# Kernel optimization log

Measured on AMD Instinct MI355X. Metric: run time of the kernel, lower is better.

The kernel has to match this reference:

```python
import jax, jax.numpy as jnp
import numpy as np

B, T, C = 4, 2048, 1024
H = 16
D = C // H  # head_dim = 64


def setup_inputs() -> dict:
    key = jax.random.key(0)
    k1, k2, k3 = jax.random.split(key, 3)
    x = jax.random.normal(k1, (B, T, C), dtype=jnp.float32)
    w_qkv = jax.random.normal(k2, (C, 3 * C), dtype=jnp.float32) * (C ** -0.5)
    b_qkv = jnp.zeros((3 * C,), dtype=jnp.float32)
    w_proj = jax.random.normal(k3, (C, C), dtype=jnp.float32) * (C ** -0.5)
    b_proj = jnp.zeros((C,), dtype=jnp.float32)
    return {"x": x, "w_qkv": w_qkv, "b_qkv": b_qkv, "w_proj": w_proj, "b_proj": b_proj}


def reference(x, w_qkv, b_qkv, w_proj, b_proj):
    # qkv projection: (B,T,C) -> (B,T,3,H,D) -> q,k,v each (B,H,T,D)
    qkv = (x @ w_qkv + b_qkv).reshape(B, T, 3, H, D)
    q, k, v = jnp.moveaxis(qkv, 2, 0)           # each (B, T, H, D)
    q = q.transpose(0, 2, 1, 3)                 # (B, H, T, D)
    k = k.transpose(0, 2, 1, 3)
    v = v.transpose(0, 2, 1, 3)

    scale = 1.0 / jnp.sqrt(jnp.float32(D))
    attn = jnp.einsum('bhqd,bhkd->bhqk', q, k) * scale  # (B,H,T,T)
    causal = jnp.tril(jnp.ones((T, T), dtype=bool))
    attn = jnp.where(causal[None, None], attn, -jnp.inf)
    attn = jax.nn.softmax(attn, axis=-1)
    # dropout p=0.0 (eval mode) -> identity
    out = jnp.einsum('bhqk,bhkd->bhqd', attn, v)        # (B,H,T,D)
    out = out.transpose(0, 2, 1, 3).reshape(B, T, C)
    return out @ w_proj + b_proj
```

## Files before the change

kernel.cpp:

```cpp
#include <hip/hip_runtime.h>
#include <hip/hip_bf16.h>


#define Bsz 4
#define Tsz 2048
#define Csz 1024
#define Hn  16
#define Dh  64

typedef unsigned short u16;
typedef __attribute__((ext_vector_type(8))) short bf16x8;
typedef __attribute__((ext_vector_type(4))) float f32x4;
typedef __attribute__((ext_vector_type(4))) unsigned int u32x4;
typedef __attribute__((ext_vector_type(2))) unsigned int u32x2;

__device__ __forceinline__ u16 f2b(float f) {
  __hip_bfloat16 h = __float2bfloat16(f);
  return *reinterpret_cast<u16*>(&h);
}

__device__ __forceinline__ unsigned pk2(float lo, float hi) {
  return __builtin_amdgcn_perm(__float_as_uint(hi) + 0x8000u,
                               __float_as_uint(lo) + 0x8000u, 0x07060302u);
}

#if __has_builtin(__builtin_amdgcn_exp2f)
#define EX2(x) __builtin_amdgcn_exp2f(x)
#else
#define EX2(x) exp2f(x)
#endif

__device__ __forceinline__ void gld_lds16(const void* g, void* lds) {
  __builtin_amdgcn_global_load_lds(
      (const __attribute__((address_space(1))) unsigned int*)g,
      (__attribute__((address_space(3))) unsigned int*)lds, 16, 0, 0);
}

__global__ __launch_bounds__(256) void cvt_f32_bf16(const float* __restrict__ in,
                                                    u16* __restrict__ out) {
  size_t i = ((size_t)blockIdx.x * 256 + threadIdx.x) * 8;
  f32x4 a = *(const f32x4*)(in + i);
  f32x4 b = *(const f32x4*)(in + i + 4);
  u16 r[8];
#pragma unroll
  for (int j = 0; j < 4; ++j) { r[j] = f2b(a[j]); r[4 + j] = f2b(b[j]); }
  *(u32x4*)(out + i) = *(const u32x4*)r;
}

__global__ __launch_bounds__(256) void cvt_transpose(const float* __restrict__ in,
                                                     u16* __restrict__ out,
                                                     int R, int C) {
  __shared__ u16 tile[64 * 66];
  const int r0 = blockIdx.x * 64, c0 = blockIdx.y * 64;
  const int tid = threadIdx.x;
#pragma unroll
  for (int i = 0; i < 16; ++i) {
    int idx = i * 256 + tid;
    int r = idx >> 6, c = idx & 63;
    tile[r * 66 + c] = f2b(in[(size_t)(r0 + r) * C + (c0 + c)]);
  }
  __syncthreads();
#pragma unroll
  for (int i = 0; i < 16; ++i) {
    int idx = i * 256 + tid;
    int c = idx >> 6, r = idx & 63;
    out[(size_t)(c0 + c) * R + (r0 + r)] = tile[r * 66 + c];
  }
}

__device__ __forceinline__ void gemm_tile_acc(const u16* __restrict__ A,
                                              const u16* __restrict__ Bt,
                                              int m0, int n0,
                                              u16* Als, u16* Bls,
                                              f32x4 acc[4][2]) {
  const int tid = threadIdx.x;
  const int w = tid >> 6, lane = tid & 63;
  const int wm = w & 1, wn = w >> 1;
  const int col = lane & 15, quad = lane >> 4;
#pragma unroll
  for (int mt = 0; mt < 4; ++mt)
#pragma unroll
    for (int nt = 0; nt < 2; ++nt)
      acc[mt][nt] = (f32x4){0.f, 0.f, 0.f, 0.f};

  const u16* asrc[2];
  const u16* bsrc[2];
#pragma unroll
  for (int c = 0; c < 2; ++c) {
    int slot = c * 512 + tid;
    int trow = slot >> 3, seg = slot & 7;
    size_t off = (size_t)trow * 1024 + (size_t)((seg ^ (trow & 7)) * 8);
    asrc[c] = A + (size_t)m0 * 1024 + off;
    bsrc[c] = Bt + (size_t)n0 * 1024 + off;
  }
  const int swz = col & 7;
  const int o0 = ((0 + quad) ^ swz) * 8;
  const int o1 = ((4 + quad) ^ swz) * 8;

#pragma unroll
  for (int c = 0; c < 2; ++c) {
    gld_lds16(asrc[c], (char*)Als + (size_t)(c * 512 + w * 64) * 16);
    gld_lds16(bsrc[c], (char*)Bls + (size_t)(c * 512 + w * 64) * 16);
    asrc[c] += 64; bsrc[c] += 64;
  }

  const int nkt = 1024 / 64;
  for (int t = 0; t < nkt; ++t) {
    asm volatile("s_waitcnt vmcnt(0)" ::: "memory");
    __builtin_amdgcn_s_barrier();
    __builtin_amdgcn_sched_barrier(0);
    const int cur = t & 1;
    if (t + 1 < nkt) {
      const int nxt = cur ^ 1;
      u16* Ad = Als + nxt * 8192;
      u16* Bd = Bls + nxt * 8192;
#pragma unroll
      for (int c = 0; c < 2; ++c) {
        gld_lds16(asrc[c], (char*)Ad + (size_t)(c * 512 + w * 64) * 16);
        gld_lds16(bsrc[c], (char*)Bd + (size_t)(c * 512 + w * 64) * 16);
        asrc[c] += 64; bsrc[c] += 64;
      }
    }
    const u16* Ac = Als + cur * 8192;
    const u16* Bc = Bls + cur * 8192;
    bf16x8 af[4][2], bfr[2][2];
#pragma unroll
    for (int mt = 0; mt < 4; ++mt) {
      const u16* r = Ac + (size_t)(wm * 64 + mt * 16 + col) * 64;
      af[mt][0] = *(const bf16x8*)(r + o0);
      af[mt][1] = *(const bf16x8*)(r + o1);
    }
#pragma unroll
    for (int nt = 0; nt < 2; ++nt) {
      const u16* r = Bc + (size_t)(wn * 32 + nt * 16 + col) * 64;
      bfr[nt][0] = *(const bf16x8*)(r + o0);
      bfr[nt][1] = *(const bf16x8*)(r + o1);
    }
#pragma unroll
    for (int kk = 0; kk < 2; ++kk)
#pragma unroll
      for (int mt = 0; mt < 4; ++mt)
#pragma unroll
        for (int nt = 0; nt < 2; ++nt)
          acc[mt][nt] = __builtin_amdgcn_mfma_f32_16x16x32_bf16(
              af[mt][kk], bfr[nt][kk], acc[mt][nt], 0, 0, 0);
  }
}

__global__ __launch_bounds__(512, 4) void gemm_qkv(const u16* __restrict__ X,
                                                   const u16* __restrict__ WT,
                                                   const float* __restrict__ bias,
                                                   u16* __restrict__ Q,
                                                   u16* __restrict__ Kc,
                                                   u16* __restrict__ Vt) {
  __shared__ __align__(16) u16 Als[2 * 128 * 64];
  __shared__ __align__(16) u16 Bls[2 * 128 * 64];
  f32x4 acc[4][2];
  const int m0 = blockIdx.x * 128, n0 = blockIdx.y * 128;
  gemm_tile_acc(X, WT, m0, n0, Als, Bls, acc);

  const float qscale = 0.18033688011112042f;
  const int tid = threadIdx.x;
  const int w = tid >> 6, lane = tid & 63;
  const int wm = w & 1, wn = w >> 1;
  const int col = lane & 15, quad = lane >> 4;
#pragma unroll
  for (int mt = 0; mt < 4; ++mt)
#pragma unroll
    for (int nt = 0; nt < 2; ++nt) {
      int n = n0 + wn * 32 + nt * 16 + col;
      int s = n >> 10, hh = (n >> 6) & (Hn - 1), d = n & 63;
      int mBase = m0 + wm * 64 + mt * 16 + quad * 4;
      int b = mBase >> 11, t0 = mBase & (Tsz - 1);
      if (s == 2) {
        u16 vals[4];
#pragma unroll
        for (int r = 0; r < 4; ++r) vals[r] = f2b(acc[mt][nt][r] + bias[n]);
        *(u32x2*)(Vt + ((size_t)(b * Hn + hh) * Dh + d) * Tsz + t0) =
            *(const u32x2*)vals;
      } else {
        const float scl = (s == 0) ? qscale : 1.f;
        u16* dst = (s == 0) ? Q : Kc;
#pragma unroll
        for (int r = 0; r < 4; ++r)
          dst[((size_t)(b * Hn + hh) * Tsz + (t0 + r)) * Dh + d] =
              f2b((acc[mt][nt][r] + bias[n]) * scl);
      }
    }
}

__global__ __launch_bounds__(512, 4) void gemm_proj(const u16* __restrict__ O,
                                                    const u16* __restrict__ WT,
                                                    const float* __restrict__ bias,
                                                    float* __restrict__ out) {
  __shared__ __align__(16) u16 Als[2 * 128 * 64];
  __shared__ __align__(16) u16 Bls[2 * 128 * 64];
  f32x4 acc[4][2];
  const int m0 = blockIdx.x * 128, n0 = blockIdx.y * 128;
  gemm_tile_acc(O, WT, m0, n0, Als, Bls, acc);

  const int tid = threadIdx.x;
  const int w = tid >> 6, lane = tid & 63;
  const int wm = w & 1, wn = w >> 1;
  const int col = lane & 15, quad = lane >> 4;
#pragma unroll
  for (int mt = 0; mt < 4; ++mt)
#pragma unroll
    for (int nt = 0; nt < 2; ++nt)
#pragma unroll
      for (int r = 0; r < 4; ++r) {
        int m = m0 + wm * 64 + mt * 16 + quad * 4 + r;
        int n = n0 + wn * 32 + nt * 16 + col;
        out[(size_t)m * Csz + n] = acc[mt][nt][r] + bias[n];
      }
}

__device__ __forceinline__ void attn_tile_stage(
    const u16* __restrict__ Kc, const u16* __restrict__ Vc,
    const bf16x8* aq, f32x4* oacc, float* lsum,
    bool domask, int rel, int qg, int col, int quad, int off0, int off1) {
  f32x4 sacc[4];
#pragma unroll
  for (int kt = 0; kt < 4; ++kt) sacc[kt] = (f32x4){0.f, 0.f, 0.f, 0.f};
#pragma unroll
  for (int ks = 0; ks < 2; ++ks)
#pragma unroll
    for (int kt = 0; kt < 4; ++kt) {
      bf16x8 bk = *(const bf16x8*)(&Kc[(kt * 16 + col) * 64 + (ks ? off1 : off0)]);
      sacc[kt] = __builtin_amdgcn_mfma_f32_16x16x32_bf16(bk, aq[ks],
                                                         sacc[kt], 0, 0, 0);
    }

  float e[4][4];
  if (domask) {
#pragma unroll
    for (int kt = 0; kt < 4; ++kt)
#pragma unroll
      for (int r = 0; r < 4; ++r) {
        int kl = rel + kt * 16 + quad * 4 + r;
        float p = (kl > qg) ? 0.f : EX2(sacc[kt][r]);
        lsum[kt] += p;
        e[kt][r] = p;
      }
  } else {
#pragma unroll
    for (int kt = 0; kt < 4; ++kt)
#pragma unroll
      for (int r = 0; r < 4; ++r) {
        float p = EX2(sacc[kt][r]);
        lsum[kt] += p;
        e[kt][r] = p;
      }
  }

#pragma unroll
  for (int ksg = 0; ksg < 2; ++ksg) {
    unsigned w00 = pk2(e[2 * ksg][0], e[2 * ksg][1]);
    unsigned w01 = pk2(e[2 * ksg][2], e[2 * ksg][3]);
    unsigned w10 = pk2(e[2 * ksg + 1][0], e[2 * ksg + 1][1]);
    unsigned w11 = pk2(e[2 * ksg + 1][2], e[2 * ksg + 1][3]);
    auto ra = __builtin_amdgcn_permlane32_swap(w00, w10, false, false);
    auto rb = __builtin_amdgcn_permlane32_swap(w01, w11, false, false);
    auto sa = __builtin_amdgcn_permlane16_swap(ra[0], ra[1], false, false);
    auto sb = __builtin_amdgcn_permlane16_swap(rb[0], rb[1], false, false);
    union { unsigned u[4]; bf16x8 v; } pf;
    pf.u[0] = sa[0]; pf.u[1] = sb[0]; pf.u[2] = sa[1]; pf.u[3] = sb[1];
#pragma unroll
    for (int dt = 0; dt < 4; ++dt) {
      bf16x8 bv = *(const bf16x8*)(&Vc[(dt * 16 + col) * 64 + (ksg ? off1 : off0)]);
      oacc[dt] = __builtin_amdgcn_mfma_f32_16x16x32_bf16(bv, pf.v,
                                                         oacc[dt], 0, 0, 0);
    }
  }
}

__global__ __launch_bounds__(512, 4) void attn(const u16* __restrict__ Q,
                                               const u16* __restrict__ Kg,
                                               const u16* __restrict__ Vt,
                                               u16* __restrict__ O) {
  __shared__ __align__(16) u16 Ks[3][64 * 64];
  __shared__ __align__(16) u16 Vs[3][64 * 64];

  const int d0 = blockIdx.x;
  const int xcd = d0 & 7;
  const int idx = d0 >> 3;
  const int bh = ((idx & 7) << 3) | xcd;
  const int a = idx >> 3;
  const int qlo = a, qhi = 15 - a;
  const int h = bh & (Hn - 1), b = bh >> 4;

  const int tid = threadIdx.x, w = tid >> 6, lane = tid & 63;
  const int col = lane & 15, quad = lane >> 4;
  const int qbl = qlo << 7, qbh = qhi << 7;

  const u16* Kbase = Kg + (size_t)bh * Tsz * Dh;
  const u16* Vbase = Vt + (size_t)bh * Dh * Tsz;

  const int trow = tid >> 3;
  const int xseg = ((tid & 7) ^ (trow & 7)) * 8;
  const size_t koff = (size_t)trow * 64 + xseg;
  const size_t voff = (size_t)trow * Tsz + xseg;
  const int swz = col & 7;
  const int off0 = ((0 + quad) ^ swz) << 3;
  const int off1 = ((4 + quad) ^ swz) << 3;

  bf16x8 aq_hi[2], aq_lo[2];
  {
    const u16* Qh = Q + ((size_t)bh * Tsz + qbh) * Dh;
    const u16* Ql = Q + ((size_t)bh * Tsz + qbl) * Dh;
#pragma unroll
    for (int ks = 0; ks < 2; ++ks) {
      aq_hi[ks] = *(const bf16x8*)(Qh + (size_t)(w * 16 + col) * Dh + ks * 32 + quad * 8);
      aq_lo[ks] = *(const bf16x8*)(Ql + (size_t)(w * 16 + col) * Dh + ks * 32 + quad * 8);
    }
  }
  asm volatile("s_waitcnt vmcnt(0)" ::: "memory");

  const int nst = 2 * qhi + 2;
  gld_lds16(Kbase + koff, &Ks[0][w * 512]);
  gld_lds16(Vbase + voff, &Vs[0][w * 512]);
  gld_lds16(Kbase + 4096 + koff, &Ks[1][w * 512]);
  gld_lds16(Vbase + 64 + voff, &Vs[1][w * 512]);

  f32x4 oacc_hi[4], oacc_lo[4];
#pragma unroll
  for (int dt = 0; dt < 4; ++dt) {
    oacc_hi[dt] = (f32x4){0.f, 0.f, 0.f, 0.f};
    oacc_lo[dt] = (f32x4){0.f, 0.f, 0.f, 0.f};
  }
  float lsum_hi[4] = {0.f, 0.f, 0.f, 0.f};
  float lsum_lo[4] = {0.f, 0.f, 0.f, 0.f};

  const u16* kdma = Kbase + 2 * 4096 + koff;
  const u16* vdma = Vbase + 2 * 64 + voff;

  const int qg = w * 16 + col;
  const int wge4 = (w >= 4) ? 1 : 0;
  const int smask_hi = 2 * qhi + wge4;
  const int smask_lo = 2 * qlo + wge4;
  const int lo_end = 2 * qlo + 1 + wge4;
  const int hi2 = 2 * qhi, lo2 = 2 * qlo;

  int cur = 0;
  for (int s = 0; s < nst; ++s) {
    if (s + 1 < nst) {
      asm volatile("s_waitcnt vmcnt(2)" ::: "memory");
    } else {
      asm volatile("s_waitcnt vmcnt(0)" ::: "memory");
    }
    __builtin_amdgcn_s_barrier();
    __builtin_amdgcn_sched_barrier(0);
    if (s + 2 < nst) {
      int pf = cur + 2; if (pf >= 3) pf -= 3;
      gld_lds16(kdma, &Ks[pf][w * 512]);
      gld_lds16(vdma, &Vs[pf][w * 512]);
      kdma += 4096;
      vdma += 64;
    }
    const u16* Kc = &Ks[cur][0];
    const u16* Vc = &Vs[cur][0];

    if (w >= 4 || s < nst - 1)
      attn_tile_stage(Kc, Vc, aq_hi, oacc_hi, lsum_hi,
                      s >= smask_hi, (s - hi2) * 64, qg, col, quad, off0, off1);
    if (s < lo_end)
      attn_tile_stage(Kc, Vc, aq_lo, oacc_lo, lsum_lo,
                      s >= smask_lo, (s - lo2) * 64, qg, col, quad, off0, off1);

    cur += 1; if (cur >= 3) cur = 0;
  }

  float vh = (lsum_hi[0] + lsum_hi[1]) + (lsum_hi[2] + lsum_hi[3]);
  vh += __shfl_xor(vh, 16);
  vh += __shfl_xor(vh, 32);
  const float invh = 1.0f / vh;
  float vl = (lsum_lo[0] + lsum_lo[1]) + (lsum_lo[2] + lsum_lo[3]);
  vl += __shfl_xor(vl, 16);
  vl += __shfl_xor(vl, 32);
  const float invl = 1.0f / vl;

  const int rgh = qbh + w * 16 + col;
  const int rgl = qbl + w * 16 + col;
  u16* OrowH = O + (((size_t)b * Tsz + rgh) * Hn + h) * Dh;
  u16* OrowL = O + (((size_t)b * Tsz + rgl) * Hn + h) * Dh;
#pragma unroll
  for (int dt = 0; dt < 4; ++dt) {
    u16 vh4[4], vl4[4];
#pragma unroll
    for (int r = 0; r < 4; ++r) {
      vh4[r] = f2b(oacc_hi[dt][r] * invh);
      vl4[r] = f2b(oacc_lo[dt][r] * invl);
    }
    *(u32x2*)(OrowH + dt * 16 + quad * 4) = *(const u32x2*)vh4;
    *(u32x2*)(OrowL + dt * 16 + quad * 4) = *(const u32x2*)vl4;
  }
}

extern "C" void kernel_launch(void* const* d_in, const int* in_sizes, int n_in,
                              void* d_out, int out_size, void* d_ws, size_t ws_size,
                              hipStream_t stream) {
  const float* x      = (const float*)d_in[0];
  const float* w_qkv  = (const float*)d_in[1];
  const float* b_qkv  = (const float*)d_in[2];
  const float* w_proj = (const float*)d_in[3];
  const float* b_proj = (const float*)d_in[4];
  float* out = (float*)d_out;

  u16* Xb     = (u16*)d_ws;
  u16* WqkvT  = Xb + (size_t)8192 * 1024;
  u16* WprojT = WqkvT + (size_t)3072 * 1024;
  u16* Qb     = WprojT + (size_t)1024 * 1024;
  u16* Kb     = Qb + (size_t)8192 * 1024;
  u16* Ob     = Kb + (size_t)8192 * 1024;
  u16* Vtb    = (u16*)d_out;

  cvt_f32_bf16<<<4096, 256, 0, stream>>>(x, Xb);
  cvt_transpose<<<dim3(16, 48), 256, 0, stream>>>(w_qkv, WqkvT, 1024, 3072);
  cvt_transpose<<<dim3(16, 16), 256, 0, stream>>>(w_proj, WprojT, 1024, 1024);
  gemm_qkv<<<dim3(64, 24), 512, 0, stream>>>(Xb, WqkvT, b_qkv, Qb, Kb, Vtb);
  attn<<<dim3(512), 512, 0, stream>>>(Qb, Kb, Vtb, Ob);
  gemm_proj<<<dim3(64, 8), 512, 0, stream>>>(Ob, WprojT, b_proj, out);
}
```

Before: 233.4 us.

## Use 256x256 tiles with interleaved LDS prefetch for QKV GEMM

Replaces the 128x128 QKV projection GEMM with a 256x256 tile kernel where each wave computes a 128x64 sub-tile, quadrupling register accumulators. The main loop splits the k-step into four MFMA phases, interleaving the next tile's global-to-LDS loads between them, and raises MFMA priority with s_setprio. The aim is more data reuse per LDS byte and better overlap of loads with compute. In exchange occupancy drops (launch bounds 2, 128KB LDS, 384 blocks), which risks load imbalance and register spilling.

```diff
diff --git a/kernel.cpp b/kernel.cpp
--- a/kernel.cpp
+++ b/kernel.cpp
@@ -66,6 +66,176 @@
     int c = idx >> 6, r = idx & 63;
     out[(size_t)(c0 + c) * R + (r0 + r)] = tile[r * 66 + c];
   }
+}
+
+__device__ __forceinline__ void gemm256_core(const u16* __restrict__ A,
+                                             const u16* __restrict__ Bt,
+                                             int m0, int n0,
+                                             u16* Als, u16* Bls,
+                                             f32x4 acc[8][4]) {
+  const int tid = threadIdx.x;
+  const int w = tid >> 6, lane = tid & 63;
+  const int wm = w & 1, wn = w >> 1;
+  const int col = lane & 15, quad = lane >> 4;
+#pragma unroll
+  for (int mt = 0; mt < 8; ++mt)
+#pragma unroll
+    for (int nt = 0; nt < 4; ++nt)
+      acc[mt][nt] = (f32x4){0.f, 0.f, 0.f, 0.f};
+
+  const u16* aP[4];
+  const u16* bP[4];
+#pragma unroll
+  for (int c = 0; c < 4; ++c) {
+    int slot = c * 512 + tid;
+    int trow = slot >> 3, seg = slot & 7;
+    size_t off = (size_t)trow * 1024 + (size_t)((seg ^ (trow & 7)) * 8);
+    aP[c] = A + (size_t)m0 * 1024 + off;
+    bP[c] = Bt + (size_t)n0 * 1024 + off;
+  }
+  const int swz = col & 7;
+  const int o0 = ((0 + quad) ^ swz) * 8;
+  const int o1 = ((4 + quad) ^ swz) * 8;
+
+#pragma unroll
+  for (int c = 0; c < 4; ++c) {
+    gld_lds16(aP[c], Als + c * 4096 + w * 512);
+    gld_lds16(bP[c], Bls + c * 4096 + w * 512);
+    aP[c] += 64; bP[c] += 64;
+  }
+  asm volatile("s_waitcnt vmcnt(0)" ::: "memory");
+  __builtin_amdgcn_s_barrier();
+
+  const int nkt = 1024 / 64;
+  for (int t = 0; t < nkt; ++t) {
+    const int cur = t & 1, nxt = cur ^ 1;
+    const u16* Ac = Als + cur * 16384;
+    const u16* Bc = Bls + cur * 16384;
+    u16* Ad = Als + nxt * 16384;
+    u16* Bd = Bls + nxt * 16384;
+    const bool st = (t + 1 < nkt);
+
+    bf16x8 b0[4], af[4];
+#pragma unroll
+    for (int nt = 0; nt < 4; ++nt)
+      b0[nt] = *(const bf16x8*)(Bc + (size_t)(wn * 64 + nt * 16 + col) * 64 + o0);
+#pragma unroll
+    for (int mt = 0; mt < 4; ++mt)
+      af[mt] = *(const bf16x8*)(Ac + (size_t)(wm * 128 + mt * 16 + col) * 64 + o0);
+    if (st) {
+#pragma unroll
+      for (int c = 0; c < 4; ++c) {
+        gld_lds16(aP[c], Ad + c * 4096 + w * 512);
+        aP[c] += 64;
+      }
+    }
+    __builtin_amdgcn_s_barrier();
+    __builtin_amdgcn_s_setprio(1);
+#pragma unroll
+    for (int mt = 0; mt < 4; ++mt)
+#pragma unroll
+      for (int nt = 0; nt < 4; ++nt)
+        acc[mt][nt] = __builtin_amdgcn_mfma_f32_16x16x32_bf16(af[mt], b0[nt],
+                                                              acc[mt][nt], 0, 0, 0);
+    __builtin_amdgcn_s_setprio(0);
+    __builtin_amdgcn_s_barrier();
+
+#pragma unroll
+    for (int mt = 0; mt < 4; ++mt)
+      af[mt] = *(const bf16x8*)(Ac + (size_t)(wm * 128 + (mt + 4) * 16 + col) * 64 + o0);
+    if (st) {
+#pragma unroll
+      for (int c = 0; c < 4; ++c) {
+        gld_lds16(bP[c], Bd + c * 4096 + w * 512);
+        bP[c] += 64;
+      }
+    }
+    __builtin_amdgcn_s_barrier();
+    __builtin_amdgcn_s_setprio(1);
+#pragma unroll
+    for (int mt = 0; mt < 4; ++mt)
+#pragma unroll
+      for (int nt = 0; nt < 4; ++nt)
+        acc[mt + 4][nt] = __builtin_amdgcn_mfma_f32_16x16x32_bf16(af[mt], b0[nt],
+                                                                  acc[mt + 4][nt], 0, 0, 0);
+    __builtin_amdgcn_s_setprio(0);
+    __builtin_amdgcn_s_barrier();
+
+#pragma unroll
+    for (int nt = 0; nt < 4; ++nt)
+      b0[nt] = *(const bf16x8*)(Bc + (size_t)(wn * 64 + nt * 16 + col) * 64 + o1);
+#pragma unroll
+    for (int mt = 0; mt < 4; ++mt)
+      af[mt] = *(const bf16x8*)(Ac + (size_t)(wm * 128 + mt * 16 + col) * 64 + o1);
+    __builtin_amdgcn_s_barrier();
+    __builtin_amdgcn_s_setprio(1);
+#pragma unroll
+    for (int mt = 0; mt < 4; ++mt)
+#pragma unroll
+      for (int nt = 0; nt < 4; ++nt)
+        acc[mt][nt] = __builtin_amdgcn_mfma_f32_16x16x32_bf16(af[mt], b0[nt],
+                                                              acc[mt][nt], 0, 0, 0);
+    __builtin_amdgcn_s_setprio(0);
+    __builtin_amdgcn_s_barrier();
+
+#pragma unroll
+    for (int mt = 0; mt < 4; ++mt)
+      af[mt] = *(const bf16x8*)(Ac + (size_t)(wm * 128 + (mt + 4) * 16 + col) * 64 + o1);
+    __builtin_amdgcn_s_barrier();
+    __builtin_amdgcn_s_setprio(1);
+#pragma unroll
+    for (int mt = 0; mt < 4; ++mt)
+#pragma unroll
+      for (int nt = 0; nt < 4; ++nt)
+        acc[mt + 4][nt] = __builtin_amdgcn_mfma_f32_16x16x32_bf16(af[mt], b0[nt],
+                                                                  acc[mt + 4][nt], 0, 0, 0);
+    __builtin_amdgcn_s_setprio(0);
+    asm volatile("s_waitcnt vmcnt(0)" ::: "memory");
+    __builtin_amdgcn_sched_barrier(0);
+    __builtin_amdgcn_s_barrier();
+  }
+}
+
+__global__ __launch_bounds__(512, 2) void gemm_qkv(const u16* __restrict__ X,
+                                                   const u16* __restrict__ WT,
+                                                   const float* __restrict__ bias,
+                                                   u16* __restrict__ Q,
+                                                   u16* __restrict__ Kc,
+                                                   u16* __restrict__ Vt) {
+  __shared__ __align__(16) u16 Als[2 * 256 * 64];
+  __shared__ __align__(16) u16 Bls[2 * 256 * 64];
+  f32x4 acc[8][4];
+  const int m0 = blockIdx.x * 256, n0 = blockIdx.y * 256;
+  gemm256_core(X, WT, m0, n0, Als, Bls, acc);
+
+  const float qscale = 0.18033688011112042f;
+  const int tid = threadIdx.x;
+  const int w = tid >> 6, lane = tid & 63;
+  const int wm = w & 1, wn = w >> 1;
+  const int col = lane & 15, quad = lane >> 4;
+#pragma unroll
+  for (int mt = 0; mt < 8; ++mt)
+#pragma unroll
+    for (int nt = 0; nt < 4; ++nt) {
+      int n = n0 + wn * 64 + nt * 16 + col;
+      int s = n >> 10, hh = (n >> 6) & (Hn - 1), d = n & 63;
+      int mBase = m0 + wm * 128 + mt * 16 + quad * 4;
+      int b = mBase >> 11, t0 = mBase & (Tsz - 1);
+      if (s == 2) {
+        u16 vals[4];
+#pragma unroll
+        for (int r = 0; r < 4; ++r) vals[r] = f2b(acc[mt][nt][r] + bias[n]);
+        *(u32x2*)(Vt + ((size_t)(b * Hn + hh) * Dh + d) * Tsz + t0) =
+            *(const u32x2*)vals;
+      } else {
+        const float scl = (s == 0) ? qscale : 1.f;
+        u16* dst = (s == 0) ? Q : Kc;
+#pragma unroll
+        for (int r = 0; r < 4; ++r)
+          dst[((size_t)(b * Hn + hh) * Tsz + (t0 + r)) * Dh + d] =
+              f2b((acc[mt][nt][r] + bias[n]) * scl);
+      }
+    }
 }
 
 __device__ __forceinline__ void gemm_tile_acc(const u16* __restrict__ A,
@@ -145,48 +315,6 @@
           acc[mt][nt] = __builtin_amdgcn_mfma_f32_16x16x32_bf16(
               af[mt][kk], bfr[nt][kk], acc[mt][nt], 0, 0, 0);
   }
-}
-
-__global__ __launch_bounds__(512, 4) void gemm_qkv(const u16* __restrict__ X,
-                                                   const u16* __restrict__ WT,
-                                                   const float* __restrict__ bias,
-                                                   u16* __restrict__ Q,
-                                                   u16* __restrict__ Kc,
-                                                   u16* __restrict__ Vt) {
-  __shared__ __align__(16) u16 Als[2 * 128 * 64];
-  __shared__ __align__(16) u16 Bls[2 * 128 * 64];
-  f32x4 acc[4][2];
-  const int m0 = blockIdx.x * 128, n0 = blockIdx.y * 128;
-  gemm_tile_acc(X, WT, m0, n0, Als, Bls, acc);
-
-  const float qscale = 0.18033688011112042f;
-  const int tid = threadIdx.x;
-  const int w = tid >> 6, lane = tid & 63;
-  const int wm = w & 1, wn = w >> 1;
-  const int col = lane & 15, quad = lane >> 4;
-#pragma unroll
-  for (int mt = 0; mt < 4; ++mt)
-#pragma unroll
-    for (int nt = 0; nt < 2; ++nt) {
-      int n = n0 + wn * 32 + nt * 16 + col;
-      int s = n >> 10, hh = (n >> 6) & (Hn - 1), d = n & 63;
-      int mBase = m0 + wm * 64 + mt * 16 + quad * 4;
-      int b = mBase >> 11, t0 = mBase & (Tsz - 1);
-      if (s == 2) {
-        u16 vals[4];
-#pragma unroll
-        for (int r = 0; r < 4; ++r) vals[r] = f2b(acc[mt][nt][r] + bias[n]);
-        *(u32x2*)(Vt + ((size_t)(b * Hn + hh) * Dh + d) * Tsz + t0) =
-            *(const u32x2*)vals;
-      } else {
-        const float scl = (s == 0) ? qscale : 1.f;
-        u16* dst = (s == 0) ? Q : Kc;
-#pragma unroll
-        for (int r = 0; r < 4; ++r)
-          dst[((size_t)(b * Hn + hh) * Tsz + (t0 + r)) * Dh + d] =
-              f2b((acc[mt][nt][r] + bias[n]) * scl);
-      }
-    }
 }
 
 __global__ __launch_bounds__(512, 4) void gemm_proj(const u16* __restrict__ O,
@@ -417,7 +545,7 @@
   cvt_f32_bf16<<<4096, 256, 0, stream>>>(x, Xb);
   cvt_transpose<<<dim3(16, 48), 256, 0, stream>>>(w_qkv, WqkvT, 1024, 3072);
   cvt_transpose<<<dim3(16, 16), 256, 0, stream>>>(w_proj, WprojT, 1024, 1024);
-  gemm_qkv<<<dim3(64, 24), 512, 0, stream>>>(Xb, WqkvT, b_qkv, Qb, Kb, Vtb);
+  gemm_qkv<<<dim3(32, 12), 512, 0, stream>>>(Xb, WqkvT, b_qkv, Qb, Kb, Vtb);
   attn<<<dim3(512), 512, 0, stream>>>(Qb, Kb, Vtb, Ob);
   gemm_proj<<<dim3(64, 8), 512, 0, stream>>>(Ob, WprojT, b_proj, out);
 }
```

Measured after the change: 250.2 us. +7.2%, slower.
